# Optimization experiments

Hardware: AMD Instinct MI355X
Metric: run time of the kernel (lower is better)

## Reference

```python
import jax, jax.numpy as jnp
import numpy as np

ALPHA = 0.5
N_NODES = 100000
N_EDGES = 1600000
D_IN = 128
D_OUT = 128


def setup_inputs() -> dict:
    key = jax.random.key(0)
    k1, k2, k3, k4, k5, k6 = jax.random.split(key, 6)
    x = jax.random.normal(k1, (N_NODES, D_IN), dtype=jnp.float32)
    edge_index = jax.random.randint(k2, (2, N_EDGES), 0, N_NODES, dtype=jnp.int64)
    # torch Linear default init: U(-1/sqrt(fan_in), 1/sqrt(fan_in)); scale similar here
    s = 1.0 / np.sqrt(D_IN)
    W_src = jax.random.uniform(k3, (D_OUT, D_IN), jnp.float32, -s, s)
    b_src = jax.random.uniform(k4, (D_OUT,), jnp.float32, -s, s)
    W_dst = jax.random.uniform(k5, (D_OUT, D_IN), jnp.float32, -s, s)
    b_dst = jax.random.uniform(k6, (D_OUT,), jnp.float32, -s, s)
    return {"x": x, "edge_index": edge_index, "W_src": W_src, "b_src": b_src,
            "W_dst": W_dst, "b_dst": b_dst}


def _inv_sqrt(deg):
    # deg^{-1/2} with inf -> 0 (isolated nodes)
    return jnp.where(deg > 0, jax.lax.rsqrt(jnp.maximum(deg, 1e-30)), 0.0)


def reference(x, edge_index, W_src, b_src, W_dst, b_dst):
    n = x.shape[0]
    row, col = edge_index[0], edge_index[1]
    ones = jnp.ones(row.shape[0], dtype=x.dtype)
    # degrees of directed adjacency A[row, col] = 1
    deg_out = jax.ops.segment_sum(ones, row, num_segments=n)  # row sums
    deg_in = jax.ops.segment_sum(ones, col, num_segments=n)   # col sums
    # D_out^{-1/2} A D_in^{-1/2} edge weights; transpose norm yields the SAME weights
    w = _inv_sqrt(deg_out)[row] * _inv_sqrt(deg_in)[col]      # [E]
    # adj_norm @ x : aggregate sources (col) into destinations (row)
    agg_fwd = jax.ops.segment_sum(w[:, None] * x[col], row, num_segments=n)  # [N, D_IN]
    # adj_t_norm @ x : aggregate destinations (row) into sources (col)
    agg_bwd = jax.ops.segment_sum(w[:, None] * x[row], col, num_segments=n)  # [N, D_IN]
    out = ALPHA * (agg_fwd @ W_src.T + b_src) + (1.0 - ALPHA) * (agg_bwd @ W_dst.T + b_dst)
    return out
```

## Files before the change

kernel.cpp:

```cpp
#include <hip/hip_runtime.h>
#include <stdint.h>

#define D 128
#define CE 4096
#define CAP 5120

typedef __attribute__((ext_vector_type(8))) __bf16 bf16x8;
typedef __attribute__((ext_vector_type(4))) float floatx4;

union FragU { uint4 u; bf16x8 b; };

__device__ __forceinline__ float bf16_lo(uint32_t u) { return __uint_as_float(u << 16); }
__device__ __forceinline__ float bf16_hi(uint32_t u) { return __uint_as_float(u & 0xffff0000u); }
__device__ __forceinline__ uint16_t f32_to_bf16(float f) {
    uint32_t u = __float_as_uint(f);
    uint32_t r = u + 0x7fffu + ((u >> 16) & 1u);
    return (uint16_t)(r >> 16);
}
__device__ __forceinline__ uint32_t pack2(float a, float b) {
    return (uint32_t)f32_to_bf16(a) | ((uint32_t)f32_to_bf16(b) << 16);
}

__device__ __forceinline__ uint32_t block_excl_scan_256(
    uint32_t val, uint32_t* tmp4, int tid)
{
    int lane = tid & 63, wid = tid >> 6;
    uint32_t inc = val;
    #pragma unroll
    for (int off = 1; off < 64; off <<= 1) {
        uint32_t t = __shfl_up(inc, off, 64);
        if (lane >= off) inc += t;
    }
    if (lane == 63) tmp4[wid] = inc;
    __syncthreads();
    uint32_t wofs = 0;
    #pragma unroll
    for (int w = 0; w < 4; ++w) wofs += (w < wid) ? tmp4[w] : 0u;
    __syncthreads();
    return wofs + inc - val;
}

__global__ __launch_bounds__(256) void k_part(
    const int* __restrict__ ei, int E, int nbuk,
    uint32_t* __restrict__ gcursor, uint32_t* __restrict__ gpairs)
{
    __shared__ uint32_t cnt[1024];
    int nb2 = 2 * nbuk;
    for (int j = threadIdx.x; j < nb2; j += 256) cnt[j] = 0;
    __syncthreads();
    int base = blockIdx.x * CE;
    int lim = min(CE, E - base);
    for (int i = threadIdx.x; i < lim; i += 256) {
        int r = ei[base + i];
        int c = ei[E + base + i];
        atomicAdd(&cnt[r >> 8], 1u);
        atomicAdd(&cnt[nbuk + (c >> 8)], 1u);
    }
    __syncthreads();
    for (int j = threadIdx.x; j < nb2; j += 256) {
        uint32_t c2 = cnt[j];
        uint32_t pos0 = c2 ? atomicAdd(&gcursor[j], c2) : 0u;
        cnt[j] = (uint32_t)j * CAP + pos0;
    }
    __syncthreads();
    for (int i = threadIdx.x; i < lim; i += 256) {
        int r = ei[base + i];
        int c = ei[E + base + i];
        uint32_t pf = atomicAdd(&cnt[r >> 8], 1u);
        gpairs[pf] = ((uint32_t)c << 8) | (uint32_t)(r & 255);
        uint32_t pb = atomicAdd(&cnt[nbuk + (c >> 8)], 1u);
        gpairs[pb] = ((uint32_t)r << 8) | (uint32_t)(c & 255);
    }
}

__global__ __launch_bounds__(256) void k_build(
    const uint32_t* __restrict__ gpairs, const uint32_t* __restrict__ gcursor,
    int nbuk, int N,
    int* __restrict__ edata, uint32_t* __restrict__ ptrg, uint32_t* __restrict__ degg,
    float* __restrict__ inv_o, float* __restrict__ inv_i)
{
    __shared__ uint32_t hist[256], cur[256], stmp[4];
    __shared__ int sdata[CAP];
    int b = blockIdx.x;
    int dir = (b >= nbuk) ? 1 : 0;
    int node0 = (b - dir * nbuk) << 8;
    uint32_t base = (uint32_t)b * CAP;
    uint32_t cnt_b = gcursor[b];
    hist[threadIdx.x] = 0;
    __syncthreads();
    for (uint32_t i = threadIdx.x; i < cnt_b; i += 256)
        atomicAdd(&hist[gpairs[base + i] & 255u], 1u);
    __syncthreads();
    uint32_t h = hist[threadIdx.x];
    uint32_t excl = block_excl_scan_256(h, stmp, threadIdx.x);
    cur[threadIdx.x] = excl;
    int n = node0 + threadIdx.x;
    if (n < N) {
        ptrg[dir * N + n] = base + excl;
        degg[dir * N + n] = h;
        float iv = h ? rsqrtf((float)h) : 0.0f;
        if (dir == 0) inv_o[n] = iv; else inv_i[n] = iv;
    }
    __syncthreads();
    for (uint32_t i = threadIdx.x; i < cnt_b; i += 256) {
        uint32_t e = gpairs[base + i];
        uint32_t pos = atomicAdd(&cur[e & 255u], 1u);
        sdata[pos] = (int)(e >> 8);
    }
    __syncthreads();
    uint32_t c4 = cnt_b & ~3u;
    for (uint32_t i = 4 * threadIdx.x; i < c4; i += 1024) {
        *(int4*)&edata[base + i] = *(const int4*)&sdata[i];
    }
    for (uint32_t i = c4 + threadIdx.x; i < cnt_b; i += 256)
        edata[base + i] = sdata[i];
}

__global__ __launch_bounds__(256) void k_mm(
    const float* __restrict__ x,
    const float* __restrict__ Wsrc, const float* __restrict__ Wdst,
    const float* __restrict__ inv_o, const float* __restrict__ inv_i,
    uint32_t* __restrict__ u2, uint32_t* __restrict__ v2, int N)
{
    __shared__ uint4 sWf[2048];
    const int lane = threadIdx.x & 63;
    const int m16 = lane & 15;
    const int quad = lane >> 4;
    const int mat = blockIdx.x & 1;
    uint32_t* outb = mat ? v2 : u2;
    const float* inv = mat ? inv_o : inv_i;
    const float* Wm = mat ? Wdst : Wsrc;

    {
        uint32_t* sW32 = (uint32_t*)sWf;
        for (int idx = threadIdx.x; idx < 8192; idx += 256) {
            int slot = idx >> 2, j2 = idx & 3;
            int ct = slot >> 8, ks = (slot >> 6) & 3, qd = (slot >> 4) & 3, mm = slot & 15;
            const float2 w = *(const float2*)(Wm + (ct * 16 + mm) * 128 + ks * 32 + qd * 8 + 2 * j2);
            sW32[idx] = pack2(0.5f * w.x, 0.5f * w.y);
        }
    }
    __syncthreads();

    const int ntiles = (N + 15) >> 4;
    const int wslot = (blockIdx.x >> 1) * 4 + (threadIdx.x >> 6);
    const int nslot = (gridDim.x >> 1) * 4;

    int t = wslot;
    if (t < ntiles) {
        float4 P[8];
        float ivr;
        {
            int node = t * 16 + m16;
            int rowA = node < N ? node : N - 1;
            const float4* xr = (const float4*)(x + (long)rowA * 128);
            #pragma unroll
            for (int ks = 0; ks < 4; ++ks) {
                P[2 * ks]     = xr[ks * 8 + quad * 2];
                P[2 * ks + 1] = xr[ks * 8 + quad * 2 + 1];
            }
            ivr = inv[rowA];
        }
        while (true) {
            int node = t * 16 + m16;
            bool ok = (node < N);
            float iv = ivr;
            bf16x8 Xf[4];
            #pragma unroll
            for (int ks = 0; ks < 4; ++ks) {
                FragU f;
                f.u.x = pack2(P[2 * ks].x,     P[2 * ks].y);
                f.u.y = pack2(P[2 * ks].z,     P[2 * ks].w);
                f.u.z = pack2(P[2 * ks + 1].x, P[2 * ks + 1].y);
                f.u.w = pack2(P[2 * ks + 1].z, P[2 * ks + 1].w);
                Xf[ks] = f.b;
            }
            int tn = t + nslot;
            if (tn < ntiles) {
                int noden = tn * 16 + m16;
                int rowN = noden < N ? noden : N - 1;
                const float4* xrn = (const float4*)(x + (long)rowN * 128);
                #pragma unroll
                for (int ks = 0; ks < 4; ++ks) {
                    P[2 * ks]     = xrn[ks * 8 + quad * 2];
                    P[2 * ks + 1] = xrn[ks * 8 + quad * 2 + 1];
                }
                ivr = inv[rowN];
            }
            #pragma unroll
            for (int ct = 0; ct < 8; ++ct) {
                floatx4 acc = {};
                #pragma unroll
                for (int ks = 0; ks < 4; ++ks) {
                    FragU wf; wf.u = sWf[ct * 256 + ks * 64 + lane];
                    acc = __builtin_amdgcn_mfma_f32_16x16x32_bf16(wf.b, Xf[ks], acc, 0, 0, 0);
                }
                if (ok) {
                    uint2 val;
                    val.x = pack2(acc[0] * iv, acc[1] * iv);
                    val.y = pack2(acc[2] * iv, acc[3] * iv);
                    *(uint2*)(outb + (long)node * 64 + ct * 8 + quad * 2) = val;
                }
            }
            if (tn >= ntiles) break;
            t = tn;
        }
    }
}

__global__ __launch_bounds__(256) void k_gather(
    const uint32_t* __restrict__ u2, const uint32_t* __restrict__ v2,
    const int* __restrict__ edata,
    const uint32_t* __restrict__ ptrg, const uint32_t* __restrict__ degg,
    const float* __restrict__ inv_out, const float* __restrict__ inv_in,
    const float* __restrict__ bsrc, const float* __restrict__ bdst,
    float* __restrict__ out, int N, int nStart, int nEnd)
{
    const int lane = threadIdx.x & 63;
    const int h = lane >> 5;
    const int j = lane & 31;
    const float4 bs = *(const float4*)(bsrc + 4 * j);
    const float4 bd = *(const float4*)(bdst + 4 * j);
    const int wid = blockIdx.x * 4 + (threadIdx.x >> 6);
    const int nw = gridDim.x * 4;

    for (int node = nStart + wid; node < nEnd; node += nw) {
        uint32_t s0 = ptrg[node],     d0 = degg[node];
        uint32_t s1 = ptrg[N + node], d1 = degg[N + node];
        float io = inv_out[node], ii = inv_in[node];

        float f0 = 0, f1 = 0, f2 = 0, f3 = 0;
        {
            uint32_t k = 0;
            for (; k + 8 <= d0; k += 8) {
                int i0 = edata[s0 + k     + h];
                int i1 = edata[s0 + k + 2 + h];
                int i2 = edata[s0 + k + 4 + h];
                int i3 = edata[s0 + k + 6 + h];
                uint2 p0 = *(const uint2*)(u2 + (long)i0 * 64 + 2 * j);
                uint2 p1 = *(const uint2*)(u2 + (long)i1 * 64 + 2 * j);
                uint2 p2 = *(const uint2*)(u2 + (long)i2 * 64 + 2 * j);
                uint2 p3 = *(const uint2*)(u2 + (long)i3 * 64 + 2 * j);
                f0 += bf16_lo(p0.x) + bf16_lo(p1.x) + bf16_lo(p2.x) + bf16_lo(p3.x);
                f1 += bf16_hi(p0.x) + bf16_hi(p1.x) + bf16_hi(p2.x) + bf16_hi(p3.x);
                f2 += bf16_lo(p0.y) + bf16_lo(p1.y) + bf16_lo(p2.y) + bf16_lo(p3.y);
                f3 += bf16_hi(p0.y) + bf16_hi(p1.y) + bf16_hi(p2.y) + bf16_hi(p3.y);
            }
            for (; k + 2 <= d0; k += 2) {
                int i0 = edata[s0 + k + h];
                uint2 p = *(const uint2*)(u2 + (long)i0 * 64 + 2 * j);
                f0 += bf16_lo(p.x); f1 += bf16_hi(p.x);
                f2 += bf16_lo(p.y); f3 += bf16_hi(p.y);
            }
            if (k < d0 && h == 0) {
                int i0 = edata[s0 + k];
                uint2 p = *(const uint2*)(u2 + (long)i0 * 64 + 2 * j);
                f0 += bf16_lo(p.x); f1 += bf16_hi(p.x);
                f2 += bf16_lo(p.y); f3 += bf16_hi(p.y);
            }
        }

        float g0 = 0, g1 = 0, g2 = 0, g3 = 0;
        {
            uint32_t k = 0;
            for (; k + 8 <= d1; k += 8) {
                int i0 = edata[s1 + k     + h];
                int i1 = edata[s1 + k + 2 + h];
                int i2 = edata[s1 + k + 4 + h];
                int i3 = edata[s1 + k + 6 + h];
                uint2 p0 = *(const uint2*)(v2 + (long)i0 * 64 + 2 * j);
                uint2 p1 = *(const uint2*)(v2 + (long)i1 * 64 + 2 * j);
                uint2 p2 = *(const uint2*)(v2 + (long)i2 * 64 + 2 * j);
                uint2 p3 = *(const uint2*)(v2 + (long)i3 * 64 + 2 * j);
                g0 += bf16_lo(p0.x) + bf16_lo(p1.x) + bf16_lo(p2.x) + bf16_lo(p3.x);
                g1 += bf16_hi(p0.x) + bf16_hi(p1.x) + bf16_hi(p2.x) + bf16_hi(p3.x);
                g2 += bf16_lo(p0.y) + bf16_lo(p1.y) + bf16_lo(p2.y) + bf16_lo(p3.y);
                g3 += bf16_hi(p0.y) + bf16_hi(p1.y) + bf16_hi(p2.y) + bf16_hi(p3.y);
            }
            for (; k + 2 <= d1; k += 2) {
                int i0 = edata[s1 + k + h];
                uint2 p = *(const uint2*)(v2 + (long)i0 * 64 + 2 * j);
                g0 += bf16_lo(p.x); g1 += bf16_hi(p.x);
                g2 += bf16_lo(p.y); g3 += bf16_hi(p.y);
            }
            if (k < d1 && h == 0) {
                int i0 = edata[s1 + k];
                uint2 p = *(const uint2*)(v2 + (long)i0 * 64 + 2 * j);
                g0 += bf16_lo(p.x); g1 += bf16_hi(p.x);
                g2 += bf16_lo(p.y); g3 += bf16_hi(p.y);
            }
        }

        f0 += __shfl_xor(f0, 32); f1 += __shfl_xor(f1, 32);
        f2 += __shfl_xor(f2, 32); f3 += __shfl_xor(f3, 32);
        g0 += __shfl_xor(g0, 32); g1 += __shfl_xor(g1, 32);
        g2 += __shfl_xor(g2, 32); g3 += __shfl_xor(g3, 32);

        if (h == 0) {
            float4 o;
            o.x = io * f0 + ii * g0 + 0.5f * (bs.x + bd.x);
            o.y = io * f1 + ii * g1 + 0.5f * (bs.y + bd.y);
            o.z = io * f2 + ii * g2 + 0.5f * (bs.z + bd.z);
            o.w = io * f3 + ii * g3 + 0.5f * (bs.w + bd.w);
            *(float4*)(out + (long)node * 128 + 4 * j) = o;
        }
    }
}

extern "C" void kernel_launch(void* const* d_in, const int* in_sizes, int n_in,
                              void* d_out, int out_size, void* d_ws, size_t ws_size,
                              hipStream_t stream) {
    const int N = in_sizes[0] / D;
    const int E = in_sizes[1] / 2;
    const int nbuk = (N + 255) >> 8;
    const int nb2 = 2 * nbuk;

    const float* x    = (const float*)d_in[0];
    const int*   ei   = (const int*)d_in[1];
    const float* Wsrc = (const float*)d_in[2];
    const float* bsrc = (const float*)d_in[3];
    const float* Wdst = (const float*)d_in[4];
    const float* bdst = (const float*)d_in[5];

    char* ws = (char*)d_ws;
    size_t off = 0;
    uint32_t* gcur   = (uint32_t*)(ws + off); off += 1024 * 4;
    float*    inv_o  = (float*)(ws + off);    off += (size_t)N * 4;
    float*    inv_i  = (float*)(ws + off);    off += (size_t)N * 4;
    uint32_t* ptrg   = (uint32_t*)(ws + off); off += (size_t)2 * N * 4;
    uint32_t* degg   = (uint32_t*)(ws + off); off += (size_t)2 * N * 4;
    uint32_t* gpairs = (uint32_t*)(ws + off); off += (size_t)nb2 * CAP * 4;
    int*      edata  = (int*)(ws + off);      off += (size_t)nb2 * CAP * 4;
    uint32_t* u2     = (uint32_t*)(ws + off); off += (size_t)N * 64 * 4;
    uint32_t* v2     = (uint32_t*)(ws + off); off += (size_t)N * 64 * 4;

    hipMemsetAsync(gcur, 0, (size_t)nb2 * 4, stream);

    k_part<<<(E + CE - 1) / CE, 256, 0, stream>>>(ei, E, nbuk, gcur, gpairs);

    k_build<<<nb2, 256, 0, stream>>>(gpairs, gcur, nbuk, N,
                                     edata, ptrg, degg, inv_o, inv_i);

    k_mm<<<1024, 256, 0, stream>>>(x, Wsrc, Wdst, inv_o, inv_i, u2, v2, N);

    k_gather<<<2048, 256, 0, stream>>>(u2, v2, edata, ptrg, degg,
                                       inv_o, inv_i, bsrc, bdst,
                                       (float*)d_out, N, 0, N);
}
```

Before: 315.5 us.

## Replace bucketed two-pass CSR build with global-atomic degree count and scatter

Replaces the bucket-partition plus per-bucket shared-memory sort CSR construction with three simple kernels: per-node degree counting with global atomics, a per-bucket scan to compute row pointers, and a scatter that places each edge via per-node global atomic cursors. This removes the intermediate gpairs buffer and its extra read/write pass. The cost is many contended global atomics and uncoalesced scattered writes, and edge order within a node becomes nondeterministic. It also swaps the hand-written bf16 packing for the HIP intrinsic conversion in the matmul kernel.

```diff
diff --git a/kernel.cpp b/kernel.cpp
--- a/kernel.cpp
+++ b/kernel.cpp
@@ -1,8 +1,8 @@
 #include <hip/hip_runtime.h>
+#include <hip/hip_bf16.h>
 #include <stdint.h>
 
 #define D 128
-#define CE 4096
 #define CAP 5120
 
 typedef __attribute__((ext_vector_type(8))) __bf16 bf16x8;
@@ -19,6 +19,10 @@
 }
 __device__ __forceinline__ uint32_t pack2(float a, float b) {
     return (uint32_t)f32_to_bf16(a) | ((uint32_t)f32_to_bf16(b) << 16);
+}
+__device__ __forceinline__ uint32_t pk2(float a, float b) {
+    __hip_bfloat162 h = __float22bfloat162_rn(make_float2(a, b));
+    return *reinterpret_cast<uint32_t*>(&h);
 }
 
 __device__ __forceinline__ uint32_t block_excl_scan_256(
@@ -40,80 +44,52 @@
     return wofs + inc - val;
 }
 
-__global__ __launch_bounds__(256) void k_part(
-    const int* __restrict__ ei, int E, int nbuk,
-    uint32_t* __restrict__ gcursor, uint32_t* __restrict__ gpairs)
-{
-    __shared__ uint32_t cnt[1024];
-    int nb2 = 2 * nbuk;
-    for (int j = threadIdx.x; j < nb2; j += 256) cnt[j] = 0;
-    __syncthreads();
-    int base = blockIdx.x * CE;
-    int lim = min(CE, E - base);
-    for (int i = threadIdx.x; i < lim; i += 256) {
-        int r = ei[base + i];
-        int c = ei[E + base + i];
-        atomicAdd(&cnt[r >> 8], 1u);
-        atomicAdd(&cnt[nbuk + (c >> 8)], 1u);
-    }
-    __syncthreads();
-    for (int j = threadIdx.x; j < nb2; j += 256) {
-        uint32_t c2 = cnt[j];
-        uint32_t pos0 = c2 ? atomicAdd(&gcursor[j], c2) : 0u;
-        cnt[j] = (uint32_t)j * CAP + pos0;
-    }
-    __syncthreads();
-    for (int i = threadIdx.x; i < lim; i += 256) {
-        int r = ei[base + i];
-        int c = ei[E + base + i];
-        uint32_t pf = atomicAdd(&cnt[r >> 8], 1u);
-        gpairs[pf] = ((uint32_t)c << 8) | (uint32_t)(r & 255);
-        uint32_t pb = atomicAdd(&cnt[nbuk + (c >> 8)], 1u);
-        gpairs[pb] = ((uint32_t)r << 8) | (uint32_t)(c & 255);
-    }
-}
-
-__global__ __launch_bounds__(256) void k_build(
-    const uint32_t* __restrict__ gpairs, const uint32_t* __restrict__ gcursor,
-    int nbuk, int N,
-    int* __restrict__ edata, uint32_t* __restrict__ ptrg, uint32_t* __restrict__ degg,
+__global__ __launch_bounds__(256) void k_deg(
+    const int* __restrict__ ei, int E, int N, uint32_t* __restrict__ degg)
+{
+    int i = threadIdx.x + blockIdx.x * 256;
+    int stride = gridDim.x * 256;
+    for (; i < E; i += stride) {
+        int r = ei[i], c = ei[E + i];
+        atomicAdd(&degg[r], 1u);
+        atomicAdd(&degg[N + c], 1u);
+    }
+}
+
+__global__ __launch_bounds__(256) void k_ptr(
+    const uint32_t* __restrict__ degg, int nbuk, int N,
+    uint32_t* __restrict__ ptrg, uint32_t* __restrict__ curg,
     float* __restrict__ inv_o, float* __restrict__ inv_i)
 {
-    __shared__ uint32_t hist[256], cur[256], stmp[4];
-    __shared__ int sdata[CAP];
+    __shared__ uint32_t stmp[4];
     int b = blockIdx.x;
     int dir = (b >= nbuk) ? 1 : 0;
     int node0 = (b - dir * nbuk) << 8;
     uint32_t base = (uint32_t)b * CAP;
-    uint32_t cnt_b = gcursor[b];
-    hist[threadIdx.x] = 0;
-    __syncthreads();
-    for (uint32_t i = threadIdx.x; i < cnt_b; i += 256)
-        atomicAdd(&hist[gpairs[base + i] & 255u], 1u);
-    __syncthreads();
-    uint32_t h = hist[threadIdx.x];
+    int n = node0 + threadIdx.x;
+    uint32_t h = (n < N) ? degg[dir * N + n] : 0u;
     uint32_t excl = block_excl_scan_256(h, stmp, threadIdx.x);
-    cur[threadIdx.x] = excl;
-    int n = node0 + threadIdx.x;
     if (n < N) {
         ptrg[dir * N + n] = base + excl;
-        degg[dir * N + n] = h;
+        curg[dir * N + n] = base + excl;
         float iv = h ? rsqrtf((float)h) : 0.0f;
         if (dir == 0) inv_o[n] = iv; else inv_i[n] = iv;
     }
-    __syncthreads();
-    for (uint32_t i = threadIdx.x; i < cnt_b; i += 256) {
-        uint32_t e = gpairs[base + i];
-        uint32_t pos = atomicAdd(&cur[e & 255u], 1u);
-        sdata[pos] = (int)(e >> 8);
-    }
-    __syncthreads();
-    uint32_t c4 = cnt_b & ~3u;
-    for (uint32_t i = 4 * threadIdx.x; i < c4; i += 1024) {
-        *(int4*)&edata[base + i] = *(const int4*)&sdata[i];
-    }
-    for (uint32_t i = c4 + threadIdx.x; i < cnt_b; i += 256)
-        edata[base + i] = sdata[i];
+}
+
+__global__ __launch_bounds__(256) void k_scatter(
+    const int* __restrict__ ei, int E, int N,
+    uint32_t* __restrict__ curg, int* __restrict__ edata)
+{
+    int i = threadIdx.x + blockIdx.x * 256;
+    int stride = gridDim.x * 256;
+    for (; i < E; i += stride) {
+        int r = ei[i], c = ei[E + i];
+        uint32_t p0 = atomicAdd(&curg[r], 1u);
+        edata[p0] = c;
+        uint32_t p1 = atomicAdd(&curg[N + c], 1u);
+        edata[p1] = r;
+    }
 }
 
 __global__ __launch_bounds__(256) void k_mm(
@@ -169,10 +145,10 @@
             #pragma unroll
             for (int ks = 0; ks < 4; ++ks) {
                 FragU f;
-                f.u.x = pack2(P[2 * ks].x,     P[2 * ks].y);
-                f.u.y = pack2(P[2 * ks].z,     P[2 * ks].w);
-                f.u.z = pack2(P[2 * ks + 1].x, P[2 * ks + 1].y);
-                f.u.w = pack2(P[2 * ks + 1].z, P[2 * ks + 1].w);
+                f.u.x = pk2(P[2 * ks].x,     P[2 * ks].y);
+                f.u.y = pk2(P[2 * ks].z,     P[2 * ks].w);
+                f.u.z = pk2(P[2 * ks + 1].x, P[2 * ks + 1].y);
+                f.u.w = pk2(P[2 * ks + 1].z, P[2 * ks + 1].w);
                 Xf[ks] = f.b;
             }
             int tn = t + nslot;
@@ -197,8 +173,8 @@
                 }
                 if (ok) {
                     uint2 val;
-                    val.x = pack2(acc[0] * iv, acc[1] * iv);
-                    val.y = pack2(acc[2] * iv, acc[3] * iv);
+                    val.x = pk2(acc[0] * iv, acc[1] * iv);
+                    val.y = pk2(acc[2] * iv, acc[3] * iv);
                     *(uint2*)(outb + (long)node * 64 + ct * 8 + quad * 2) = val;
                 }
             }
@@ -324,22 +300,22 @@
 
     char* ws = (char*)d_ws;
     size_t off = 0;
-    uint32_t* gcur   = (uint32_t*)(ws + off); off += 1024 * 4;
     float*    inv_o  = (float*)(ws + off);    off += (size_t)N * 4;
     float*    inv_i  = (float*)(ws + off);    off += (size_t)N * 4;
     uint32_t* ptrg   = (uint32_t*)(ws + off); off += (size_t)2 * N * 4;
     uint32_t* degg   = (uint32_t*)(ws + off); off += (size_t)2 * N * 4;
-    uint32_t* gpairs = (uint32_t*)(ws + off); off += (size_t)nb2 * CAP * 4;
+    uint32_t* curg   = (uint32_t*)(ws + off); off += (size_t)2 * N * 4;
     int*      edata  = (int*)(ws + off);      off += (size_t)nb2 * CAP * 4;
     uint32_t* u2     = (uint32_t*)(ws + off); off += (size_t)N * 64 * 4;
     uint32_t* v2     = (uint32_t*)(ws + off); off += (size_t)N * 64 * 4;
 
-    hipMemsetAsync(gcur, 0, (size_t)nb2 * 4, stream);
-
-    k_part<<<(E + CE - 1) / CE, 256, 0, stream>>>(ei, E, nbuk, gcur, gpairs);
-
-    k_build<<<nb2, 256, 0, stream>>>(gpairs, gcur, nbuk, N,
-                                     edata, ptrg, degg, inv_o, inv_i);
+    hipMemsetAsync(degg, 0, (size_t)2 * N * 4, stream);
+
+    k_deg<<<2048, 256, 0, stream>>>(ei, E, N, degg);
+
+    k_ptr<<<nb2, 256, 0, stream>>>(degg, nbuk, N, ptrg, curg, inv_o, inv_i);
+
+    k_scatter<<<2048, 256, 0, stream>>>(ei, E, N, curg, edata);
 
     k_mm<<<1024, 256, 0, stream>>>(x, Wsrc, Wdst, inv_o, inv_i, u2, v2, N);
 
```

Result: slower. 657.3 us (+108.3%).
